# Optimization experiments

Measured on AMD Instinct MI355X. Metric: run time of the kernel, lower is better.

The kernel has to match this reference:

```python
import jax, jax.numpy as jnp
import numpy as np

N_EXC = 512
N_INH = 128
N_TOTAL = N_EXC + N_INH  # 640
N_IN = 16
N_OUT = 2
BATCH = 64
T = 1000
ALPHA = 25.0 / 50.0       # dt / tau
NOISE_SCALE = 0.01


def setup_inputs() -> dict:
    key = jax.random.key(0)
    k1, k2, k3, k4 = jax.random.split(key, 4)
    inputs = jax.random.normal(k1, (BATCH, T, N_IN), dtype=jnp.float32)
    # positive raw recurrent weights, scaled ~2/N so the 1000-step recurrence is stable
    W_rec_raw = jax.random.uniform(k2, (N_TOTAL, N_TOTAL), dtype=jnp.float32) * (2.0 / N_TOTAL)
    W_in = jax.random.uniform(k3, (N_TOTAL, N_IN), dtype=jnp.float32, minval=-0.1, maxval=0.1)
    W_out = jax.random.uniform(k4, (N_OUT, N_EXC), dtype=jnp.float32, minval=-0.1, maxval=0.1)
    b_out = jnp.zeros((N_OUT,), dtype=jnp.float32)
    return {"inputs": inputs, "W_rec_raw": W_rec_raw, "W_in": W_in,
            "W_out": W_out, "b_out": b_out}


def _dale_W_rec(W_rec_raw):
    # Dale's law: columns for E units positive, columns for I units negative; zero diagonal.
    col_sign = jnp.where(jnp.arange(N_TOTAL) >= N_EXC, -1.0, 1.0)
    diag_mask = 1.0 - jnp.eye(N_TOTAL, dtype=W_rec_raw.dtype)
    return jnp.abs(W_rec_raw) * col_sign[None, :] * diag_mask


def reference(inputs, W_rec_raw, W_in, W_out, b_out):
    B, Tn, _ = inputs.shape
    W_rec = _dale_W_rec(W_rec_raw)
    # pre-generate the per-step injected noise: [T, B, N_TOTAL]
    noise = (NOISE_SCALE * jnp.sqrt(jnp.float32(ALPHA))) * jax.random.normal(
        jax.random.key(42), (Tn, B, N_TOTAL), dtype=inputs.dtype)
    u_seq = jnp.swapaxes(inputs, 0, 1)  # [T, B, N_IN]
    x0 = jnp.zeros((B, N_TOTAL), dtype=inputs.dtype)

    def step(x, scan_in):
        u_t, eps_t = scan_in
        r = jax.nn.softplus(x)                                  # rates from previous potential
        rec_in = r @ W_rec.T                                    # [B, N_TOTAL]
        ext_in = u_t @ W_in.T                                   # [B, N_TOTAL]
        x_new = (1.0 - ALPHA) * x + ALPHA * (rec_in + ext_in) + eps_t
        y = r[:, :N_EXC] @ W_out.T + b_out                      # [B, N_OUT]
        return x_new, (r, y)

    _, (rates_t, outs_t) = jax.lax.scan(step, x0, (u_seq, noise))
    rates = jnp.swapaxes(rates_t, 0, 1)   # [B, T, N_TOTAL]
    outputs = jnp.swapaxes(outs_t, 0, 1)  # [B, T, N_OUT]
    return rates, outputs
```

## Files before the change

### kernel.cpp

```cpp
#include <hip/hip_runtime.h>

#define N_EXC  512
#define NTOT   640
#define NIN    16
#define BATCH  64
#define TSTEPS 1000
#define CHUNK  160
#define NBLKG  4
#define THREADS 512
#define NPT    10
#define KPT    20
#define KREG   12
#define KLDS   8
#define RBUF_BYTES (2 * BATCH * NBLKG * CHUNK * 4)

typedef float    f32x2 __attribute__((ext_vector_type(2)));
typedef unsigned u32x4 __attribute__((ext_vector_type(4)));
typedef unsigned u32x2 __attribute__((ext_vector_type(2)));

__device__ __forceinline__ void threefry_0_42(unsigned x0, unsigned x1,
                                              unsigned& o0, unsigned& o1) {
    const unsigned ks1 = 42u;
    const unsigned ks2 = 0x1BD11BDAu ^ 42u;
    x0 += 0u; x1 += ks1;
#define TF_RND(r) { x0 += x1; x1 = (x1 << (r)) | (x1 >> (32 - (r))); x1 ^= x0; }
    TF_RND(13) TF_RND(15) TF_RND(26) TF_RND(6)
    x0 += ks1; x1 += ks2 + 1u;
    TF_RND(17) TF_RND(29) TF_RND(16) TF_RND(24)
    x0 += ks2; x1 += 0u + 2u;
    TF_RND(13) TF_RND(15) TF_RND(26) TF_RND(6)
    x0 += 0u; x1 += ks1 + 3u;
    TF_RND(17) TF_RND(29) TF_RND(16) TF_RND(24)
    x0 += ks1; x1 += ks2 + 4u;
    TF_RND(13) TF_RND(15) TF_RND(26) TF_RND(6)
    x0 += ks2; x1 += 0u + 5u;
#undef TF_RND
    o0 = x0; o1 = x1;
}

__device__ __forceinline__ unsigned jax_bits_partitionable(unsigned idx) {
    unsigned o0, o1;
    threefry_0_42(0u, idx, o0, o1);
    return o0 ^ o1;
}

__device__ __forceinline__ float noise_from_bits(unsigned bits) {
    float f = __uint_as_float(0x3f800000u | (bits >> 9)) - 1.0f;
    float u = __fadd_rn(__fmul_rn(f, 2.0f), -0.99999994f);
    u = fmaxf(-0.99999994f, u);
    float w = -log1pf(-__fmul_rn(u, u));
    float p;
    if (w < 5.0f) {
        float ww = w - 2.5f;
        p = 2.81022636e-08f;
        p = fmaf(p, ww, 3.43273939e-07f);
        p = fmaf(p, ww, -3.5233877e-06f);
        p = fmaf(p, ww, -4.39150654e-06f);
        p = fmaf(p, ww, 0.00021858087f);
        p = fmaf(p, ww, -0.00125372503f);
        p = fmaf(p, ww, -0.00417768164f);
        p = fmaf(p, ww, 0.246640727f);
        p = fmaf(p, ww, 1.50140941f);
    } else {
        float ww = sqrtf(w) - 3.0f;
        p = -0.000200214257f;
        p = fmaf(p, ww, 0.000100950558f);
        p = fmaf(p, ww, 0.00134934322f);
        p = fmaf(p, ww, -0.00367342844f);
        p = fmaf(p, ww, 0.00573950773f);
        p = fmaf(p, ww, -0.0076224613f);
        p = fmaf(p, ww, 0.00943887047f);
        p = fmaf(p, ww, 1.00167406f);
        p = fmaf(p, ww, 2.83297682f);
    }
    float z = 1.41421354f * (p * u);
    return (0.01f * 0.70710677f) * z;
}

__device__ __forceinline__ unsigned rne_bf16(float f) {
    unsigned u = __float_as_uint(f);
    return (u + 0x7FFFu + ((u >> 16) & 1u)) >> 16;
}

__device__ __forceinline__ unsigned packw2(const float* __restrict__ W,
                                           int n0, int n1, int k, float sg) {
    float lo = fabsf(W[(size_t)n0 * NTOT + k]) * sg; if (n0 == k) lo = 0.f;
    float hi = fabsf(W[(size_t)n1 * NTOT + k]) * sg; if (n1 == k) hi = 0.f;
    return rne_bf16(lo) | (rne_bf16(hi) << 16);
}

__device__ __forceinline__ f32x2 uf2(unsigned u) {
    u32x2 t = {u << 16, u & 0xFFFF0000u};
    return __builtin_bit_cast(f32x2, t);
}

#define FOR12(M) M(0) M(1) M(2) M(3) M(4) M(5) M(6) M(7) M(8) M(9) M(10) M(11)

__global__ __launch_bounds__(THREADS)
void eirnn_sync(const float* __restrict__ inputs, const float* __restrict__ Wraw,
                const float* __restrict__ W_in, const float* __restrict__ W_out,
                const float* __restrict__ b_out, float* __restrict__ rates_out,
                float* __restrict__ outs_out, unsigned* __restrict__ rbuf) {
    const int b   = blockIdx.x & 63;
    const int g   = blockIdx.x >> 6;
    const int tid = threadIdx.x;
    const int ti  = tid & 15;
    const int tj  = tid >> 4;
    const int wv  = tid >> 6;
    const int nbase = g * CHUNK;
    const int nloc  = nbase + ti * NPT;
    const int kbase = tj * KPT;

    __shared__ __align__(16) float r_all[2][NTOT];
    __shared__ __align__(8)  float part[8 * CHUNK];
    __shared__ float win_s[CHUNK * 17];
    __shared__ float wo_s[2 * N_EXC];
    __shared__ float u_s[2][NIN];
    __shared__ float red0[8], red1[8];
    __shared__ float bo_s[2];
    __shared__ u32x4    w4_lds[KLDS * THREADS];
    __shared__ unsigned w1_lds[KLDS * THREADS];

#define DECLW(K) u32x4 wA##K; unsigned wB##K;
    FOR12(DECLW)
#undef DECLW

#define LOADW(K) {                                                          \
        const int k_ = kbase + (K);                                         \
        const float sg_ = (k_ < N_EXC) ? 1.f : -1.f;                        \
        wA##K = (u32x4){packw2(Wraw, nloc + 0, nloc + 1, k_, sg_),          \
                        packw2(Wraw, nloc + 2, nloc + 3, k_, sg_),          \
                        packw2(Wraw, nloc + 4, nloc + 5, k_, sg_),          \
                        packw2(Wraw, nloc + 6, nloc + 7, k_, sg_)};         \
        wB##K = packw2(Wraw, nloc + 8, nloc + 9, k_, sg_);                  \
    }
    FOR12(LOADW)
#undef LOADW

#pragma unroll
    for (int kk = 0; kk < KLDS; ++kk) {
        const int k_ = kbase + KREG + kk;
        const float sg_ = (k_ < N_EXC) ? 1.f : -1.f;
        w4_lds[kk * THREADS + tid] =
            (u32x4){packw2(Wraw, nloc + 0, nloc + 1, k_, sg_),
                    packw2(Wraw, nloc + 2, nloc + 3, k_, sg_),
                    packw2(Wraw, nloc + 4, nloc + 5, k_, sg_),
                    packw2(Wraw, nloc + 6, nloc + 7, k_, sg_)};
        w1_lds[kk * THREADS + tid] = packw2(Wraw, nloc + 8, nloc + 9, k_, sg_);
    }

    for (int i = tid; i < CHUNK * NIN; i += THREADS) {
        int o = i >> 4, j = i & 15;
        win_s[o * 17 + j] = W_in[(nbase + o) * NIN + j];
    }
    for (int i = tid; i < 2 * N_EXC; i += THREADS) wo_s[i] = W_out[i];
    if (tid < 2) bo_s[tid] = b_out[tid];

    const float* inp_b = inputs    + (size_t)b * TSTEPS * NIN;
    float* rates_b     = rates_out + (size_t)b * TSTEPS * NTOT;
    float* outs_b      = outs_out  + (size_t)b * TSTEPS * 2;

    const int pidx = tid - 32;
    const int pp   = pidx / CHUNK;
    const int pgg  = pp + (pp >= g ? 1 : 0);
    const int po   = pidx - pp * CHUNK;

    float x = 0.0f;
    __syncthreads();

    for (int t = 0; t < TSTEPS; ++t) {
        const int buf = t & 1;
        const unsigned tagv = (unsigned)(t & 3);
        unsigned* rb_base = rbuf + (size_t)(buf * BATCH + b) * (NBLKG * CHUNK);

        if (tid < CHUNK) {
            float r = fmaxf(x, 0.0f) + log1pf(expf(-fabsf(x)));
            unsigned rbits = (__float_as_uint(r) & ~3u) | tagv;
            r_all[buf][nbase + tid] = __uint_as_float(rbits);
            rates_b[t * NTOT + nbase + tid] = r;
            __hip_atomic_store(rb_base + g * CHUNK + tid, rbits,
                               __ATOMIC_RELAXED, __HIP_MEMORY_SCOPE_AGENT);
        }
        if (tid >= THREADS - NIN) {
            u_s[buf][tid - (THREADS - NIN)] =
                inp_b[t * NIN + (tid - (THREADS - NIN))];
        }
        if (tid >= 32) {
            const unsigned* src = rb_base + pgg * CHUNK + po;
            unsigned w;
            do {
                w = __hip_atomic_load(src, __ATOMIC_RELAXED,
                                      __HIP_MEMORY_SCOPE_AGENT);
            } while (((w & 3u) != tagv) || ((int)w <= 0x00800000));
            r_all[buf][pgg * CHUNK + po] = __uint_as_float(w);
        }
        __syncthreads();

        {
            const float* ra = r_all[buf];
            f32x2 acc0 = {0.f, 0.f}, acc1 = {0.f, 0.f}, acc2 = {0.f, 0.f};
            f32x2 acc3 = {0.f, 0.f}, acc4 = {0.f, 0.f};
#define FMAK(K) { const float rk_ = ra[kbase + (K)];                        \
                  acc0 += uf2(wA##K.x) * rk_;                               \
                  acc1 += uf2(wA##K.y) * rk_;                               \
                  acc2 += uf2(wA##K.z) * rk_;                               \
                  acc3 += uf2(wA##K.w) * rk_;                               \
                  acc4 += uf2(wB##K)   * rk_; }
            FOR12(FMAK)
#undef FMAK
#pragma unroll
            for (int kk = 0; kk < KLDS; ++kk) {
                const float rk_ = ra[kbase + KREG + kk];
                u32x4 wa = w4_lds[kk * THREADS + tid];
                unsigned wb = w1_lds[kk * THREADS + tid];
                acc0 += uf2(wa.x) * rk_;
                acc1 += uf2(wa.y) * rk_;
                acc2 += uf2(wa.z) * rk_;
                acc3 += uf2(wa.w) * rk_;
                acc4 += uf2(wb)   * rk_;
            }
#define WRED(S) { S.x += __shfl_xor(S.x, 16); S.x += __shfl_xor(S.x, 32);   \
                  S.y += __shfl_xor(S.y, 16); S.y += __shfl_xor(S.y, 32); }
            WRED(acc0) WRED(acc1) WRED(acc2) WRED(acc3) WRED(acc4)
#undef WRED
            if ((tid & 63) < 16) {
                float* pq = &part[wv * CHUNK + (tid & 15) * NPT];
                *(f32x2*)(pq + 0) = acc0;
                *(f32x2*)(pq + 2) = acc1;
                *(f32x2*)(pq + 4) = acc2;
                *(f32x2*)(pq + 6) = acc3;
                *(f32x2*)(pq + 8) = acc4;
            }
            if (g == 0) {
                float rr = r_all[buf][tid];
                float p0 = rr * wo_s[tid], p1 = rr * wo_s[N_EXC + tid];
#pragma unroll
                for (int off = 32; off; off >>= 1) {
                    p0 += __shfl_down(p0, off);
                    p1 += __shfl_down(p1, off);
                }
                if ((tid & 63) == 0) { red0[wv] = p0; red1[wv] = p1; }
            }
        }
        __syncthreads();

        if (tid < CHUNK) {
            float rec = 0.0f;
#pragma unroll
            for (int j = 0; j < 8; ++j) rec += part[j * CHUNK + tid];
            float ext = 0.0f;
#pragma unroll
            for (int j = 0; j < NIN; ++j)
                ext = fmaf(win_s[tid * 17 + j], u_s[buf][j], ext);
            unsigned idx = (unsigned)(t * (BATCH * NTOT) + b * NTOT + (nbase + tid));
            float eps = noise_from_bits(jax_bits_partitionable(idx));
            x = (0.5f * x + 0.5f * (rec + ext)) + eps;
        }
        if (g == 0 && tid == 0) {
            float y0 = bo_s[0], y1 = bo_s[1];
#pragma unroll
            for (int k = 0; k < 8; ++k) { y0 += red0[k]; y1 += red1[k]; }
            outs_b[t * 2 + 0] = y0;
            outs_b[t * 2 + 1] = y1;
        }
    }
}

extern "C" void kernel_launch(void* const* d_in, const int* in_sizes, int n_in,
                              void* d_out, int out_size, void* d_ws, size_t ws_size,
                              hipStream_t stream) {
    const float* inputs = (const float*)d_in[0];
    const float* Wraw   = (const float*)d_in[1];
    const float* W_in   = (const float*)d_in[2];
    const float* W_out  = (const float*)d_in[3];
    const float* b_out  = (const float*)d_in[4];

    float* out   = (float*)d_out;
    float* rates = out;
    float* outs  = out + (size_t)BATCH * TSTEPS * NTOT;

    unsigned* rbuf = (unsigned*)d_ws;

    hipMemsetAsync(d_ws, 0xAA, RBUF_BYTES, stream);
    eirnn_sync<<<dim3(NBLKG * BATCH), dim3(THREADS), 0, stream>>>(
        inputs, Wraw, W_in, W_out, b_out, rates, outs, rbuf);
}
```

Measured before the change: 3.046 ms.

## Overlap local-chunk GEMV with cross-block rate exchange wait

Reorders the recurrent weight partition so each block first computes the GEMV slice for its own locally produced rates, then spins on the other blocks' rates. The global rates store and the next-step input load are moved after the exchange barrier. The intent is to hide inter-block synchronization latency behind useful FMA work. In exchange it adds one extra __syncthreads per step and changes the summation order of the accumulation.

```diff
diff --git a/kernel.cpp b/kernel.cpp
--- a/kernel.cpp
+++ b/kernel.cpp
@@ -9,9 +9,6 @@
 #define NBLKG  4
 #define THREADS 512
 #define NPT    10
-#define KPT    20
-#define KREG   12
-#define KLDS   8
 #define RBUF_BYTES (2 * BATCH * NBLKG * CHUNK * 4)
 
 typedef float    f32x2 __attribute__((ext_vector_type(2)));
@@ -94,8 +91,6 @@
     return __builtin_bit_cast(f32x2, t);
 }
 
-#define FOR12(M) M(0) M(1) M(2) M(3) M(4) M(5) M(6) M(7) M(8) M(9) M(10) M(11)
-
 __global__ __launch_bounds__(THREADS)
 void eirnn_sync(const float* __restrict__ inputs, const float* __restrict__ Wraw,
                 const float* __restrict__ W_in, const float* __restrict__ W_out,
@@ -109,7 +104,6 @@
     const int wv  = tid >> 6;
     const int nbase = g * CHUNK;
     const int nloc  = nbase + ti * NPT;
-    const int kbase = tj * KPT;
 
     __shared__ __align__(16) float r_all[2][NTOT];
     __shared__ __align__(8)  float part[8 * CHUNK];
@@ -118,36 +112,41 @@
     __shared__ float u_s[2][NIN];
     __shared__ float red0[8], red1[8];
     __shared__ float bo_s[2];
-    __shared__ u32x4    w4_lds[KLDS * THREADS];
-    __shared__ unsigned w1_lds[KLDS * THREADS];
-
-#define DECLW(K) u32x4 wA##K; unsigned wB##K;
-    FOR12(DECLW)
-#undef DECLW
-
-#define LOADW(K) {                                                          \
-        const int k_ = kbase + (K);                                         \
-        const float sg_ = (k_ < N_EXC) ? 1.f : -1.f;                        \
-        wA##K = (u32x4){packw2(Wraw, nloc + 0, nloc + 1, k_, sg_),          \
-                        packw2(Wraw, nloc + 2, nloc + 3, k_, sg_),          \
-                        packw2(Wraw, nloc + 4, nloc + 5, k_, sg_),          \
-                        packw2(Wraw, nloc + 6, nloc + 7, k_, sg_)};         \
-        wB##K = packw2(Wraw, nloc + 8, nloc + 9, k_, sg_);                  \
-    }
-    FOR12(LOADW)
-#undef LOADW
-
-#pragma unroll
-    for (int kk = 0; kk < KLDS; ++kk) {
-        const int k_ = kbase + KREG + kk;
-        const float sg_ = (k_ < N_EXC) ? 1.f : -1.f;
-        w4_lds[kk * THREADS + tid] =
-            (u32x4){packw2(Wraw, nloc + 0, nloc + 1, k_, sg_),
-                    packw2(Wraw, nloc + 2, nloc + 3, k_, sg_),
-                    packw2(Wraw, nloc + 4, nloc + 5, k_, sg_),
-                    packw2(Wraw, nloc + 6, nloc + 7, k_, sg_)};
-        w1_lds[kk * THREADS + tid] = packw2(Wraw, nloc + 8, nloc + 9, k_, sg_);
-    }
+    __shared__ u32x4    w4_lds[8 * THREADS];
+    __shared__ unsigned w1_lds[8 * THREADS];
+
+#define DECLSLOT(J) u32x4 wA##J##0, wA##J##1, wA##J##2; \
+                    unsigned wB##J##0, wB##J##1, wB##J##2;
+    DECLSLOT(0) DECLSLOT(1) DECLSLOT(2) DECLSLOT(3)
+#undef DECLSLOT
+
+#define MAKE4(K_, SG_) (u32x4){packw2(Wraw, nloc + 0, nloc + 1, K_, SG_),   \
+                               packw2(Wraw, nloc + 2, nloc + 3, K_, SG_),   \
+                               packw2(Wraw, nloc + 4, nloc + 5, K_, SG_),   \
+                               packw2(Wraw, nloc + 6, nloc + 7, K_, SG_)}
+#define LOADSLOT(J) {                                                       \
+        const int cb_ = ((g + (J)) & 3) * CHUNK + tj * 5;                   \
+        { const int k_ = cb_ + 0; const float sg_ = (k_ < N_EXC) ? 1.f : -1.f; \
+          wA##J##0 = MAKE4(k_, sg_);                                        \
+          wB##J##0 = packw2(Wraw, nloc + 8, nloc + 9, k_, sg_); }           \
+        { const int k_ = cb_ + 1; const float sg_ = (k_ < N_EXC) ? 1.f : -1.f; \
+          wA##J##1 = MAKE4(k_, sg_);                                        \
+          wB##J##1 = packw2(Wraw, nloc + 8, nloc + 9, k_, sg_); }           \
+        { const int k_ = cb_ + 2; const float sg_ = (k_ < N_EXC) ? 1.f : -1.f; \
+          wA##J##2 = MAKE4(k_, sg_);                                        \
+          wB##J##2 = packw2(Wraw, nloc + 8, nloc + 9, k_, sg_); }           \
+        { const int k_ = cb_ + 3; const float sg_ = (k_ < N_EXC) ? 1.f : -1.f; \
+          w4_lds[((J) * 2 + 0) * THREADS + tid] = MAKE4(k_, sg_);           \
+          w1_lds[((J) * 2 + 0) * THREADS + tid] =                           \
+              packw2(Wraw, nloc + 8, nloc + 9, k_, sg_); }                  \
+        { const int k_ = cb_ + 4; const float sg_ = (k_ < N_EXC) ? 1.f : -1.f; \
+          w4_lds[((J) * 2 + 1) * THREADS + tid] = MAKE4(k_, sg_);           \
+          w1_lds[((J) * 2 + 1) * THREADS + tid] =                           \
+              packw2(Wraw, nloc + 8, nloc + 9, k_, sg_); }                  \
+    }
+    LOADSLOT(0) LOADSLOT(1) LOADSLOT(2) LOADSLOT(3)
+#undef LOADSLOT
+#undef MAKE4
 
     for (int i = tid; i < CHUNK * NIN; i += THREADS) {
         int o = i >> 4, j = i & 15;
@@ -165,6 +164,9 @@
     const int pgg  = pp + (pp >= g ? 1 : 0);
     const int po   = pidx - pp * CHUNK;
 
+    if (tid >= THREADS - NIN)
+        u_s[0][tid - (THREADS - NIN)] = inp_b[tid - (THREADS - NIN)];
+
     float x = 0.0f;
     __syncthreads();
 
@@ -172,75 +174,86 @@
         const int buf = t & 1;
         const unsigned tagv = (unsigned)(t & 3);
         unsigned* rb_base = rbuf + (size_t)(buf * BATCH + b) * (NBLKG * CHUNK);
-
+        const float* ra = r_all[buf];
+
+        float r_exact = 0.0f;
         if (tid < CHUNK) {
-            float r = fmaxf(x, 0.0f) + log1pf(expf(-fabsf(x)));
-            unsigned rbits = (__float_as_uint(r) & ~3u) | tagv;
+            r_exact = fmaxf(x, 0.0f) + log1pf(expf(-fabsf(x)));
+            unsigned rbits = (__float_as_uint(r_exact) & ~3u) | tagv;
             r_all[buf][nbase + tid] = __uint_as_float(rbits);
-            rates_b[t * NTOT + nbase + tid] = r;
             __hip_atomic_store(rb_base + g * CHUNK + tid, rbits,
                                __ATOMIC_RELAXED, __HIP_MEMORY_SCOPE_AGENT);
         }
-        if (tid >= THREADS - NIN) {
-            u_s[buf][tid - (THREADS - NIN)] =
-                inp_b[t * NIN + (tid - (THREADS - NIN))];
-        }
+        __syncthreads();
+
+        const unsigned* psrc = rb_base + pgg * CHUNK + po;
+        unsigned wspec = 0u;
+        if (tid >= 32)
+            wspec = __hip_atomic_load(psrc, __ATOMIC_RELAXED,
+                                      __HIP_MEMORY_SCOPE_AGENT);
+
+        f32x2 acc0 = {0.f, 0.f}, acc1 = {0.f, 0.f}, acc2 = {0.f, 0.f};
+        f32x2 acc3 = {0.f, 0.f}, acc4 = {0.f, 0.f};
+#define FMA5(WA, WB, RK) { acc0 += uf2((WA).x) * (RK);                      \
+                           acc1 += uf2((WA).y) * (RK);                      \
+                           acc2 += uf2((WA).z) * (RK);                      \
+                           acc3 += uf2((WA).w) * (RK);                      \
+                           acc4 += uf2(WB)     * (RK); }
+#define GEMV_SLOT(J) {                                                      \
+        const float* rc_ = ra + (((g + (J)) & 3) * CHUNK + tj * 5);         \
+        const float r0_ = rc_[0], r1_ = rc_[1], r2_ = rc_[2];               \
+        const float r3_ = rc_[3], r4_ = rc_[4];                             \
+        FMA5(wA##J##0, wB##J##0, r0_)                                       \
+        FMA5(wA##J##1, wB##J##1, r1_)                                       \
+        FMA5(wA##J##2, wB##J##2, r2_)                                       \
+        { u32x4 wa_ = w4_lds[((J) * 2 + 0) * THREADS + tid];                \
+          unsigned wb_ = w1_lds[((J) * 2 + 0) * THREADS + tid];             \
+          FMA5(wa_, wb_, r3_) }                                             \
+        { u32x4 wa_ = w4_lds[((J) * 2 + 1) * THREADS + tid];                \
+          unsigned wb_ = w1_lds[((J) * 2 + 1) * THREADS + tid];             \
+          FMA5(wa_, wb_, r4_) }                                             \
+    }
+        GEMV_SLOT(0)
+
         if (tid >= 32) {
-            const unsigned* src = rb_base + pgg * CHUNK + po;
-            unsigned w;
-            do {
-                w = __hip_atomic_load(src, __ATOMIC_RELAXED,
+            unsigned w = wspec;
+            while (((w & 3u) != tagv) || ((int)w <= 0x00800000)) {
+                w = __hip_atomic_load(psrc, __ATOMIC_RELAXED,
                                       __HIP_MEMORY_SCOPE_AGENT);
-            } while (((w & 3u) != tagv) || ((int)w <= 0x00800000));
+            }
             r_all[buf][pgg * CHUNK + po] = __uint_as_float(w);
         }
         __syncthreads();
 
-        {
-            const float* ra = r_all[buf];
-            f32x2 acc0 = {0.f, 0.f}, acc1 = {0.f, 0.f}, acc2 = {0.f, 0.f};
-            f32x2 acc3 = {0.f, 0.f}, acc4 = {0.f, 0.f};
-#define FMAK(K) { const float rk_ = ra[kbase + (K)];                        \
-                  acc0 += uf2(wA##K.x) * rk_;                               \
-                  acc1 += uf2(wA##K.y) * rk_;                               \
-                  acc2 += uf2(wA##K.z) * rk_;                               \
-                  acc3 += uf2(wA##K.w) * rk_;                               \
-                  acc4 += uf2(wB##K)   * rk_; }
-            FOR12(FMAK)
-#undef FMAK
-#pragma unroll
-            for (int kk = 0; kk < KLDS; ++kk) {
-                const float rk_ = ra[kbase + KREG + kk];
-                u32x4 wa = w4_lds[kk * THREADS + tid];
-                unsigned wb = w1_lds[kk * THREADS + tid];
-                acc0 += uf2(wa.x) * rk_;
-                acc1 += uf2(wa.y) * rk_;
-                acc2 += uf2(wa.z) * rk_;
-                acc3 += uf2(wa.w) * rk_;
-                acc4 += uf2(wb)   * rk_;
-            }
+        if (tid < CHUNK) rates_b[t * NTOT + nbase + tid] = r_exact;
+        if (tid >= THREADS - NIN && t + 1 < TSTEPS)
+            u_s[(t + 1) & 1][tid - (THREADS - NIN)] =
+                inp_b[(t + 1) * NIN + (tid - (THREADS - NIN))];
+
+        GEMV_SLOT(1) GEMV_SLOT(2) GEMV_SLOT(3)
+#undef GEMV_SLOT
+#undef FMA5
 #define WRED(S) { S.x += __shfl_xor(S.x, 16); S.x += __shfl_xor(S.x, 32);   \
                   S.y += __shfl_xor(S.y, 16); S.y += __shfl_xor(S.y, 32); }
-            WRED(acc0) WRED(acc1) WRED(acc2) WRED(acc3) WRED(acc4)
+        WRED(acc0) WRED(acc1) WRED(acc2) WRED(acc3) WRED(acc4)
 #undef WRED
-            if ((tid & 63) < 16) {
-                float* pq = &part[wv * CHUNK + (tid & 15) * NPT];
-                *(f32x2*)(pq + 0) = acc0;
-                *(f32x2*)(pq + 2) = acc1;
-                *(f32x2*)(pq + 4) = acc2;
-                *(f32x2*)(pq + 6) = acc3;
-                *(f32x2*)(pq + 8) = acc4;
+        if ((tid & 63) < 16) {
+            float* pq = &part[wv * CHUNK + (tid & 15) * NPT];
+            *(f32x2*)(pq + 0) = acc0;
+            *(f32x2*)(pq + 2) = acc1;
+            *(f32x2*)(pq + 4) = acc2;
+            *(f32x2*)(pq + 6) = acc3;
+            *(f32x2*)(pq + 8) = acc4;
+        }
+        if (g == 0) {
+            float rr = r_all[buf][tid];
+            float p0 = rr * wo_s[tid], p1 = rr * wo_s[N_EXC + tid];
+#pragma unroll
+            for (int off = 32; off; off >>= 1) {
+                p0 += __shfl_down(p0, off);
+                p1 += __shfl_down(p1, off);
             }
-            if (g == 0) {
-                float rr = r_all[buf][tid];
-                float p0 = rr * wo_s[tid], p1 = rr * wo_s[N_EXC + tid];
-#pragma unroll
-                for (int off = 32; off; off >>= 1) {
-                    p0 += __shfl_down(p0, off);
-                    p1 += __shfl_down(p1, off);
-                }
-                if ((tid & 63) == 0) { red0[wv] = p0; red1[wv] = p1; }
-            }
+            if ((tid & 63) == 0) { red0[wv] = p0; red1[wv] = p1; }
         }
         __syncthreads();
 
```

After: 3.075 ms. About the same (+0.9%).

## Split neurons into eight chunks per block and process two batch rows per block

Applied to the files above, without the earlier changes.

Reworks the partitioning so each of 256 blocks owns 80 neurons for two batch rows, with 1024 threads. Each thread holds only five bf16 weight columns in registers, which removes the LDS weight spill, and it reuses each weight for both batch rows. W_in is packed to bf16, W_out is kept in registers, and the rates store, input prefetch and noise generation move after the barrier. The cost is that each block must poll more rows from the cross-block exchange buffer, and the gather now spans eight producer blocks per batch row instead of four, which adds synchronisation latency per step.

```diff
diff --git a/kernel.cpp b/kernel.cpp
--- a/kernel.cpp
+++ b/kernel.cpp
@@ -5,14 +5,11 @@
 #define NIN    16
 #define BATCH  64
 #define TSTEPS 1000
-#define CHUNK  160
-#define NBLKG  4
-#define THREADS 512
+#define CHUNK  80
+#define THREADS 1024
 #define NPT    10
-#define KPT    20
-#define KREG   12
-#define KLDS   8
-#define RBUF_BYTES (2 * BATCH * NBLKG * CHUNK * 4)
+#define KPT    5
+#define RBUF_BYTES (2 * BATCH * NTOT * 4)
 
 typedef float    f32x2 __attribute__((ext_vector_type(2)));
 typedef unsigned u32x4 __attribute__((ext_vector_type(4)));
@@ -94,35 +91,34 @@
     return __builtin_bit_cast(f32x2, t);
 }
 
-#define FOR12(M) M(0) M(1) M(2) M(3) M(4) M(5) M(6) M(7) M(8) M(9) M(10) M(11)
-
-__global__ __launch_bounds__(THREADS)
+#define FOR5(M) M(0) M(1) M(2) M(3) M(4)
+
+__global__ __launch_bounds__(THREADS, 4)
 void eirnn_sync(const float* __restrict__ inputs, const float* __restrict__ Wraw,
                 const float* __restrict__ W_in, const float* __restrict__ W_out,
                 const float* __restrict__ b_out, float* __restrict__ rates_out,
                 float* __restrict__ outs_out, unsigned* __restrict__ rbuf) {
-    const int b   = blockIdx.x & 63;
-    const int g   = blockIdx.x >> 6;
+    const int bb  = blockIdx.x & 31;
+    const int g   = blockIdx.x >> 5;
     const int tid = threadIdx.x;
-    const int ti  = tid & 15;
-    const int tj  = tid >> 4;
+    const int ti  = tid & 7;
+    const int tj  = tid >> 3;
     const int wv  = tid >> 6;
     const int nbase = g * CHUNK;
     const int nloc  = nbase + ti * NPT;
     const int kbase = tj * KPT;
 
-    __shared__ __align__(16) float r_all[2][NTOT];
-    __shared__ __align__(8)  float part[8 * CHUNK];
-    __shared__ float win_s[CHUNK * 17];
-    __shared__ float wo_s[2 * N_EXC];
-    __shared__ float u_s[2][NIN];
-    __shared__ float red0[8], red1[8];
-    __shared__ float bo_s[2];
-    __shared__ u32x4    w4_lds[KLDS * THREADS];
-    __shared__ unsigned w1_lds[KLDS * THREADS];
+    __shared__ __align__(16) float smem[21504];
+    float*    r_all = smem;
+    float*    part  = smem + 2560;
+    unsigned* win_s = (unsigned*)(smem + 5120);
+    float*    u_s   = smem + 5840;
+    float*    red0  = smem + 5904;
+    float*    red1  = smem + 5920;
+    float*    bo_s  = smem + 5936;
 
 #define DECLW(K) u32x4 wA##K; unsigned wB##K;
-    FOR12(DECLW)
+    FOR5(DECLW)
 #undef DECLW
 
 #define LOADW(K) {                                                          \
@@ -134,36 +130,49 @@
                         packw2(Wraw, nloc + 6, nloc + 7, k_, sg_)};         \
         wB##K = packw2(Wraw, nloc + 8, nloc + 9, k_, sg_);                  \
     }
-    FOR12(LOADW)
+    FOR5(LOADW)
 #undef LOADW
 
-#pragma unroll
-    for (int kk = 0; kk < KLDS; ++kk) {
-        const int k_ = kbase + KREG + kk;
-        const float sg_ = (k_ < N_EXC) ? 1.f : -1.f;
-        w4_lds[kk * THREADS + tid] =
-            (u32x4){packw2(Wraw, nloc + 0, nloc + 1, k_, sg_),
-                    packw2(Wraw, nloc + 2, nloc + 3, k_, sg_),
-                    packw2(Wraw, nloc + 4, nloc + 5, k_, sg_),
-                    packw2(Wraw, nloc + 6, nloc + 7, k_, sg_)};
-        w1_lds[kk * THREADS + tid] = packw2(Wraw, nloc + 8, nloc + 9, k_, sg_);
-    }
-
-    for (int i = tid; i < CHUNK * NIN; i += THREADS) {
-        int o = i >> 4, j = i & 15;
-        win_s[o * 17 + j] = W_in[(nbase + o) * NIN + j];
-    }
-    for (int i = tid; i < 2 * N_EXC; i += THREADS) wo_s[i] = W_out[i];
+    for (int i = tid; i < CHUNK * 8; i += THREADS) {
+        int o = i >> 3, j = i & 7;
+        float a0 = W_in[(nbase + o) * NIN + 2 * j];
+        float a1 = W_in[(nbase + o) * NIN + 2 * j + 1];
+        win_s[o * 9 + j] = rne_bf16(a0) | (rne_bf16(a1) << 16);
+    }
+    float wo0 = 0.0f, wo1 = 0.0f;
+    if (g == 0) { wo0 = W_out[tid & 511]; wo1 = W_out[N_EXC + (tid & 511)]; }
     if (tid < 2) bo_s[tid] = b_out[tid];
 
-    const float* inp_b = inputs    + (size_t)b * TSTEPS * NIN;
-    float* rates_b     = rates_out + (size_t)b * TSTEPS * NTOT;
-    float* outs_b      = outs_out  + (size_t)b * TSTEPS * 2;
-
-    const int pidx = tid - 32;
-    const int pp   = pidx / CHUNK;
-    const int pgg  = pp + (pp >= g ? 1 : 0);
-    const int po   = pidx - pp * CHUNK;
+    const int bt_own = (tid >= CHUNK) ? 1 : 0;
+    const int o_own  = tid - bt_own * CHUNK;
+    const int batch_own = bb + bt_own * 32;
+    const float* inp0 = inputs + (size_t)bb * TSTEPS * NIN;
+    const float* inp1 = inputs + (size_t)(bb + 32) * TSTEPS * NIN;
+    float* rates_own = rates_out + (size_t)batch_own * TSTEPS * NTOT + nbase + o_own;
+    float* outs_b0 = outs_out + (size_t)bb * TSTEPS * 2;
+    float* outs_b1 = outs_out + (size_t)(bb + 32) * TSTEPS * 2;
+
+    int w1bt = 0, w1off = 0, w2off = -1;
+    if (tid >= 2 * CHUNK) {
+        const int pidx = tid - 2 * CHUNK;
+        w1bt = (pidx >= 560) ? 1 : 0;
+        int rw = pidx - w1bt * 560;
+        int p = rw / CHUNK;
+        int gg = p + (p >= g ? 1 : 0);
+        w1off = gg * CHUNK + (rw - p * CHUNK);
+        if (pidx < 256) {
+            int rw2 = 864 + pidx - 560;
+            int p2 = rw2 / CHUNK;
+            int gg2 = p2 + (p2 >= g ? 1 : 0);
+            w2off = gg2 * CHUNK + (rw2 - p2 * CHUNK);
+        }
+    }
+
+    if (tid >= THREADS - 32) {
+        int j = tid - (THREADS - 32);
+        int ubt = j >> 4, uj = j & 15;
+        u_s[ubt * 16 + uj] = (ubt ? inp1 : inp0)[uj];
+    }
 
     float x = 0.0f;
     __syncthreads();
@@ -171,69 +180,87 @@
     for (int t = 0; t < TSTEPS; ++t) {
         const int buf = t & 1;
         const unsigned tagv = (unsigned)(t & 3);
-        unsigned* rb_base = rbuf + (size_t)(buf * BATCH + b) * (NBLKG * CHUNK);
-
-        if (tid < CHUNK) {
-            float r = fmaxf(x, 0.0f) + log1pf(expf(-fabsf(x)));
-            unsigned rbits = (__float_as_uint(r) & ~3u) | tagv;
-            r_all[buf][nbase + tid] = __uint_as_float(rbits);
-            rates_b[t * NTOT + nbase + tid] = r;
-            __hip_atomic_store(rb_base + g * CHUNK + tid, rbits,
+        unsigned* rb0 = rbuf + (size_t)(buf * BATCH + bb) * NTOT;
+        unsigned* rb1 = rbuf + (size_t)(buf * BATCH + bb + 32) * NTOT;
+        float* raw = r_all + buf * 2 * NTOT;
+
+        float r_exact = 0.0f;
+        if (tid < 2 * CHUNK) {
+            r_exact = fmaxf(x, 0.0f) + log1pf(expf(-fabsf(x)));
+            unsigned rbits = (__float_as_uint(r_exact) & ~3u) | tagv;
+            raw[bt_own * NTOT + nbase + o_own] = __uint_as_float(rbits);
+            __hip_atomic_store((bt_own ? rb1 : rb0) + nbase + o_own, rbits,
                                __ATOMIC_RELAXED, __HIP_MEMORY_SCOPE_AGENT);
         }
-        if (tid >= THREADS - NIN) {
-            u_s[buf][tid - (THREADS - NIN)] =
-                inp_b[t * NIN + (tid - (THREADS - NIN))];
-        }
-        if (tid >= 32) {
-            const unsigned* src = rb_base + pgg * CHUNK + po;
+        if (tid >= 2 * CHUNK) {
+            const unsigned* s1 = (w1bt ? rb1 : rb0) + w1off;
             unsigned w;
             do {
-                w = __hip_atomic_load(src, __ATOMIC_RELAXED,
+                w = __hip_atomic_load(s1, __ATOMIC_RELAXED,
                                       __HIP_MEMORY_SCOPE_AGENT);
             } while (((w & 3u) != tagv) || ((int)w <= 0x00800000));
-            r_all[buf][pgg * CHUNK + po] = __uint_as_float(w);
+            raw[w1bt * NTOT + w1off] = __uint_as_float(w);
+            if (w2off >= 0) {
+                const unsigned* s2 = rb1 + w2off;
+                do {
+                    w = __hip_atomic_load(s2, __ATOMIC_RELAXED,
+                                          __HIP_MEMORY_SCOPE_AGENT);
+                } while (((w & 3u) != tagv) || ((int)w <= 0x00800000));
+                raw[NTOT + w2off] = __uint_as_float(w);
+            }
         }
         __syncthreads();
 
+        if (tid < 2 * CHUNK) rates_own[t * NTOT] = r_exact;
+        if (tid >= THREADS - 32 && t + 1 < TSTEPS) {
+            int j = tid - (THREADS - 32);
+            int ubt = j >> 4, uj = j & 15;
+            u_s[(((t + 1) & 1) * 2 + ubt) * 16 + uj] =
+                (ubt ? inp1 : inp0)[(t + 1) * NIN + uj];
+        }
+        float eps = 0.0f;
+        if (tid < 2 * CHUNK) {
+            unsigned idx = (unsigned)(t * (BATCH * NTOT) + batch_own * NTOT
+                                      + nbase + o_own);
+            eps = noise_from_bits(jax_bits_partitionable(idx));
+        }
+
         {
-            const float* ra = r_all[buf];
-            f32x2 acc0 = {0.f, 0.f}, acc1 = {0.f, 0.f}, acc2 = {0.f, 0.f};
-            f32x2 acc3 = {0.f, 0.f}, acc4 = {0.f, 0.f};
-#define FMAK(K) { const float rk_ = ra[kbase + (K)];                        \
-                  acc0 += uf2(wA##K.x) * rk_;                               \
-                  acc1 += uf2(wA##K.y) * rk_;                               \
-                  acc2 += uf2(wA##K.z) * rk_;                               \
-                  acc3 += uf2(wA##K.w) * rk_;                               \
-                  acc4 += uf2(wB##K)   * rk_; }
-            FOR12(FMAK)
+            const float* ra0 = raw;
+            const float* ra1 = raw + NTOT;
+            f32x2 b0a0 = {0.f,0.f}, b0a1 = {0.f,0.f}, b0a2 = {0.f,0.f};
+            f32x2 b0a3 = {0.f,0.f}, b0a4 = {0.f,0.f};
+            f32x2 b1a0 = {0.f,0.f}, b1a1 = {0.f,0.f}, b1a2 = {0.f,0.f};
+            f32x2 b1a3 = {0.f,0.f}, b1a4 = {0.f,0.f};
+#define FMAK(K) { const float rk0 = ra0[kbase + (K)];                       \
+                  const float rk1 = ra1[kbase + (K)];                       \
+                  { f32x2 w_ = uf2(wA##K.x); b0a0 += w_*rk0; b1a0 += w_*rk1; } \
+                  { f32x2 w_ = uf2(wA##K.y); b0a1 += w_*rk0; b1a1 += w_*rk1; } \
+                  { f32x2 w_ = uf2(wA##K.z); b0a2 += w_*rk0; b1a2 += w_*rk1; } \
+                  { f32x2 w_ = uf2(wA##K.w); b0a3 += w_*rk0; b1a3 += w_*rk1; } \
+                  { f32x2 w_ = uf2(wB##K);   b0a4 += w_*rk0; b1a4 += w_*rk1; } }
+            FOR5(FMAK)
 #undef FMAK
-#pragma unroll
-            for (int kk = 0; kk < KLDS; ++kk) {
-                const float rk_ = ra[kbase + KREG + kk];
-                u32x4 wa = w4_lds[kk * THREADS + tid];
-                unsigned wb = w1_lds[kk * THREADS + tid];
-                acc0 += uf2(wa.x) * rk_;
-                acc1 += uf2(wa.y) * rk_;
-                acc2 += uf2(wa.z) * rk_;
-                acc3 += uf2(wa.w) * rk_;
-                acc4 += uf2(wb)   * rk_;
-            }
-#define WRED(S) { S.x += __shfl_xor(S.x, 16); S.x += __shfl_xor(S.x, 32);   \
-                  S.y += __shfl_xor(S.y, 16); S.y += __shfl_xor(S.y, 32); }
-            WRED(acc0) WRED(acc1) WRED(acc2) WRED(acc3) WRED(acc4)
+#define WRED(S) { S.x += __shfl_xor(S.x, 8); S.x += __shfl_xor(S.x, 16);    \
+                  S.x += __shfl_xor(S.x, 32);                               \
+                  S.y += __shfl_xor(S.y, 8); S.y += __shfl_xor(S.y, 16);    \
+                  S.y += __shfl_xor(S.y, 32); }
+            WRED(b0a0) WRED(b0a1) WRED(b0a2) WRED(b0a3) WRED(b0a4)
+            WRED(b1a0) WRED(b1a1) WRED(b1a2) WRED(b1a3) WRED(b1a4)
 #undef WRED
-            if ((tid & 63) < 16) {
-                float* pq = &part[wv * CHUNK + (tid & 15) * NPT];
-                *(f32x2*)(pq + 0) = acc0;
-                *(f32x2*)(pq + 2) = acc1;
-                *(f32x2*)(pq + 4) = acc2;
-                *(f32x2*)(pq + 6) = acc3;
-                *(f32x2*)(pq + 8) = acc4;
+            if ((tid & 63) < 8) {
+                float* p0 = part + (wv * 2 + 0) * CHUNK + (tid & 7) * NPT;
+                *(f32x2*)(p0 + 0) = b0a0; *(f32x2*)(p0 + 2) = b0a1;
+                *(f32x2*)(p0 + 4) = b0a2; *(f32x2*)(p0 + 6) = b0a3;
+                *(f32x2*)(p0 + 8) = b0a4;
+                float* p1 = part + (wv * 2 + 1) * CHUNK + (tid & 7) * NPT;
+                *(f32x2*)(p1 + 0) = b1a0; *(f32x2*)(p1 + 2) = b1a1;
+                *(f32x2*)(p1 + 4) = b1a2; *(f32x2*)(p1 + 6) = b1a3;
+                *(f32x2*)(p1 + 8) = b1a4;
             }
             if (g == 0) {
-                float rr = r_all[buf][tid];
-                float p0 = rr * wo_s[tid], p1 = rr * wo_s[N_EXC + tid];
+                float rr = raw[(tid >> 9) * NTOT + (tid & 511)];
+                float p0 = rr * wo0, p1 = rr * wo1;
 #pragma unroll
                 for (int off = 32; off; off >>= 1) {
                     p0 += __shfl_down(p0, off);
@@ -244,24 +271,33 @@
         }
         __syncthreads();
 
-        if (tid < CHUNK) {
+        if (tid < 2 * CHUNK) {
             float rec = 0.0f;
 #pragma unroll
-            for (int j = 0; j < 8; ++j) rec += part[j * CHUNK + tid];
+            for (int j = 0; j < 16; ++j)
+                rec += part[(j * 2 + bt_own) * CHUNK + o_own];
+            const float* ub = u_s + (buf * 2 + bt_own) * 16;
             float ext = 0.0f;
 #pragma unroll
-            for (int j = 0; j < NIN; ++j)
-                ext = fmaf(win_s[tid * 17 + j], u_s[buf][j], ext);
-            unsigned idx = (unsigned)(t * (BATCH * NTOT) + b * NTOT + (nbase + tid));
-            float eps = noise_from_bits(jax_bits_partitionable(idx));
+            for (int j = 0; j < 8; ++j) {
+                f32x2 wj = uf2(win_s[o_own * 9 + j]);
+                ext = fmaf(wj.x, ub[2 * j], fmaf(wj.y, ub[2 * j + 1], ext));
+            }
             x = (0.5f * x + 0.5f * (rec + ext)) + eps;
         }
         if (g == 0 && tid == 0) {
             float y0 = bo_s[0], y1 = bo_s[1];
 #pragma unroll
             for (int k = 0; k < 8; ++k) { y0 += red0[k]; y1 += red1[k]; }
-            outs_b[t * 2 + 0] = y0;
-            outs_b[t * 2 + 1] = y1;
+            outs_b0[t * 2 + 0] = y0;
+            outs_b0[t * 2 + 1] = y1;
+        }
+        if (g == 0 && tid == 512) {
+            float y0 = bo_s[0], y1 = bo_s[1];
+#pragma unroll
+            for (int k = 8; k < 16; ++k) { y0 += red0[k]; y1 += red1[k]; }
+            outs_b1[t * 2 + 0] = y0;
+            outs_b1[t * 2 + 1] = y1;
         }
     }
 }
@@ -282,6 +318,6 @@
     unsigned* rbuf = (unsigned*)d_ws;
 
     hipMemsetAsync(d_ws, 0xAA, RBUF_BYTES, stream);
-    eirnn_sync<<<dim3(NBLKG * BATCH), dim3(THREADS), 0, stream>>>(
+    eirnn_sync<<<dim3(256), dim3(THREADS), 0, stream>>>(
         inputs, Wraw, W_in, W_out, b_out, rates, outs, rbuf);
 }
```

Result: slower. 6.970 ms (+128.8%).
